# Performance work log

Hardware: AMD Instinct MI355X
Metric: run time of the kernel (lower is better)

Reference implementation:

```python
import jax, jax.numpy as jnp
import numpy as np

N_NODES = 100000
N_EDGES = 1600000
INPUT_DIM, HIDDEN_DIM, OUTPUT_DIM = 128, 256, 2
BN_EPS = 1e-5


def setup_inputs() -> dict:
    key = jax.random.key(0)
    ks = jax.random.split(key, 8)
    x = jax.random.normal(ks[0], (N_NODES, INPUT_DIM), jnp.float32)
    edge_index = jax.random.randint(ks[1], (2, N_EDGES), 0, N_NODES, dtype=jnp.int32).astype(jnp.int64)
    # Glorot-ish init for GCNConv weights; PyG GCNConv has bias by default.
    def glorot(k, fan_in, fan_out):
        s = jnp.sqrt(6.0 / (fan_in + fan_out))
        return jax.random.uniform(k, (fan_in, fan_out), jnp.float32, -s, s)
    return {
        "x": x,
        "edge_index": edge_index,
        "W0": glorot(ks[2], INPUT_DIM, HIDDEN_DIM),
        "b0": jnp.zeros((HIDDEN_DIM,), jnp.float32),
        "W1": glorot(ks[3], HIDDEN_DIM, HIDDEN_DIM),
        "b1": jnp.zeros((HIDDEN_DIM,), jnp.float32),
        "W2": glorot(ks[4], HIDDEN_DIM, OUTPUT_DIM),
        "b2": jnp.zeros((OUTPUT_DIM,), jnp.float32),
        "gamma0": jnp.ones((HIDDEN_DIM,), jnp.float32),
        "beta0": jnp.zeros((HIDDEN_DIM,), jnp.float32),
        "gamma1": jnp.ones((HIDDEN_DIM,), jnp.float32),
        "beta1": jnp.zeros((HIDDEN_DIM,), jnp.float32),
    }


def _gcn_norm(edge_index, num_nodes):
    # PyG gcn_norm: add self-loops, deg over destination, D^-1/2 A_hat D^-1/2
    loop = jnp.arange(num_nodes, dtype=edge_index.dtype)
    src = jnp.concatenate([edge_index[0], loop])
    dst = jnp.concatenate([edge_index[1], loop])
    deg = jax.ops.segment_sum(jnp.ones_like(dst, jnp.float32), dst, num_segments=num_nodes)
    dinv = jax.lax.rsqrt(jnp.maximum(deg, 1.0))  # deg >= 1 due to self-loops
    norm = dinv[src] * dinv[dst]  # [E + N]
    return src, dst, norm


def _gcn_conv(x, W, b, src, dst, norm, num_nodes):
    h = x @ W                          # [N, out] dense GEMM first (PyG order)
    msg = h[src] * norm[:, None]       # gather + edge scale
    out = jax.ops.segment_sum(msg, dst, num_segments=num_nodes)  # scatter-add
    return out + b


def _batchnorm(x, gamma, beta):
    # training-mode BatchNorm1d over nodes (biased variance, as torch uses for normalization)
    mean = jnp.mean(x, axis=0)
    var = jnp.mean(jnp.square(x - mean), axis=0)
    return (x - mean) * jax.lax.rsqrt(var + BN_EPS) * gamma + beta


def reference(x, edge_index, W0, b0, W1, b1, W2, b2, gamma0, beta0, gamma1, beta1):
    n = x.shape[0]
    src, dst, norm = _gcn_norm(edge_index, n)
    h = _gcn_conv(x, W0, b0, src, dst, norm, n)
    h = jax.nn.relu(_batchnorm(h, gamma0, beta0))  # dropout is identity (eval / deterministic)
    h = _gcn_conv(h, W1, b1, src, dst, norm, n)
    h = jax.nn.relu(_batchnorm(h, gamma1, beta1))
    out = _gcn_conv(h, W2, b2, src, dst, norm, n)
    return out
```

## Files before the change

kernel.cpp:

```cpp
#include <hip/hip_runtime.h>
#include <hip/hip_fp16.h>


#define BN_EPS 1e-5f

union HF4 { float4 f; __half2 h[4]; };

typedef __attribute__((ext_vector_type(8))) _Float16 f16x8;
typedef __attribute__((ext_vector_type(4))) float f32x4;

__global__ void detect_i64(const unsigned int* __restrict__ w, int* flag) {
  __shared__ unsigned int red[256];
  unsigned int v = 0;
  int t = threadIdx.x;
  for (int i = t; i < 1024; i += 256) v |= w[2 * i + 1];
  red[t] = v;
  __syncthreads();
  for (int s = 128; s > 0; s >>= 1) {
    if (t < s) red[t] |= red[t + s];
    __syncthreads();
  }
  if (t == 0) *flag = (red[0] == 0u) ? 1 : 0;
}

__global__ void convert_deg(const unsigned int* __restrict__ w, const int* __restrict__ flag,
                            int* __restrict__ srcI, int* __restrict__ dstI,
                            int* __restrict__ deg, int E) {
  int i = blockIdx.x * blockDim.x + threadIdx.x;
  if (i >= E) return;
  int f = *flag;
  int s = (int)(f ? w[2 * (size_t)i] : w[i]);
  int d = (int)(f ? w[2 * ((size_t)E + i)] : w[(size_t)E + i]);
  srcI[i] = s;
  dstI[i] = d;
  atomicAdd(&deg[d], 1);
}

__global__ void make_dinv(const int* __restrict__ deg, float* __restrict__ dinv,
                          float* __restrict__ stats, int N) {
  int i = blockIdx.x * blockDim.x + threadIdx.x;
  if (i < 512) stats[i] = 0.f;
  if (i < N) dinv[i] = rsqrtf((float)deg[i] + 1.0f);
}

__global__ void scan_partial(const int* __restrict__ deg, int* __restrict__ blksum, int N) {
  __shared__ int s[256];
  int b = blockIdx.x, t = threadIdx.x;
  int base = b * 1024 + t * 4;
  int v = 0;
#pragma unroll
  for (int k = 0; k < 4; ++k) {
    int i = base + k;
    if (i < N) v += deg[i];
  }
  s[t] = v;
  __syncthreads();
  for (int st = 128; st > 0; st >>= 1) {
    if (t < st) s[t] += s[t + st];
    __syncthreads();
  }
  if (t == 0) blksum[b] = s[0];
}

__global__ void scan_blk(int* __restrict__ blksum, int B) {
  __shared__ int s[256];
  int t = threadIdx.x;
  int v = (t < B) ? blksum[t] : 0;
  s[t] = v;
  __syncthreads();
  for (int off = 1; off < 256; off <<= 1) {
    int u = (t >= off) ? s[t - off] : 0;
    __syncthreads();
    s[t] += u;
    __syncthreads();
  }
  if (t < B) blksum[t] = s[t] - v;
}

__global__ void scan_final(const int* __restrict__ deg, const int* __restrict__ blkoff,
                           int* __restrict__ rowptr, int N, int E) {
  __shared__ int s[256];
  int b = blockIdx.x, t = threadIdx.x;
  int base = b * 1024 + t * 4;
  int v[4];
  int sum = 0;
#pragma unroll
  for (int k = 0; k < 4; ++k) {
    int i = base + k;
    v[k] = (i < N) ? deg[i] : 0;
    sum += v[k];
  }
  s[t] = sum;
  __syncthreads();
  for (int off = 1; off < 256; off <<= 1) {
    int u = (t >= off) ? s[t - off] : 0;
    __syncthreads();
    s[t] += u;
    __syncthreads();
  }
  int ex = s[t] - sum + blkoff[b];
#pragma unroll
  for (int k = 0; k < 4; ++k) {
    int i = base + k;
    if (i < N) {
      rowptr[i] = ex;
      ex += v[k];
    }
  }
  if (b == 0 && t == 0) rowptr[N] = E;
}

__global__ void csr_scatter(const int* __restrict__ src, const int* __restrict__ dst,
                            const float* __restrict__ dinv, const int* __restrict__ rowptr,
                            int* __restrict__ fill, int* __restrict__ col,
                            float* __restrict__ wgt, int E) {
  int e = blockIdx.x * blockDim.x + threadIdx.x;
  if (e >= E) return;
  int s = src[e], d = dst[e];
  int pos = atomicAdd(&fill[d], 1);
  int slot = rowptr[d] + pos;
  col[slot] = s;
  wgt[slot] = dinv[s] * dinv[d];
}

__global__ void f32_to_f16(const float4* __restrict__ in, float4* __restrict__ outh, long n8) {
  long t = (long)blockIdx.x * blockDim.x + threadIdx.x;
  if (t >= n8) return;
  float4 a = in[2 * t], b = in[2 * t + 1];
  HF4 o;
  o.h[0] = __floats2half2_rn(a.x, a.y);
  o.h[1] = __floats2half2_rn(a.z, a.w);
  o.h[2] = __floats2half2_rn(b.x, b.y);
  o.h[3] = __floats2half2_rn(b.z, b.w);
  outh[t] = o.f;
}

__global__ void pack_w(const float* __restrict__ W, _Float16* __restrict__ Wp, int K, int NC) {
  int idx = blockIdx.x * blockDim.x + threadIdx.x;
  if (idx >= K * NC) return;
  int k = idx / NC, n = idx - k * NC;
  int kb = k >> 5, kk = k & 31, seg = kk >> 3, j = kk & 7;
  Wp[(((kb * 4 + seg) * NC) + n) * 8 + j] = (_Float16)W[idx];
}

template <int LPN, bool BN>
__global__ void agg_gather_h(const float4* __restrict__ inh, float4* __restrict__ outh,
                             const int* __restrict__ rowptr, const int* __restrict__ col,
                             const float* __restrict__ wgt, const float* __restrict__ dinv,
                             const float* __restrict__ scale, const float* __restrict__ shift,
                             int N) {
  long g = (long)blockIdx.x * blockDim.x + threadIdx.x;
  int n = (int)(g / LPN);
  int lane = (int)(g & (LPN - 1));
  if (n >= N) return;
  float sc[8], sh[8];
  if (BN) {
    int c0 = lane * 8;
#pragma unroll
    for (int i = 0; i < 8; ++i) {
      sc[i] = scale[c0 + i];
      sh[i] = shift[c0 + i];
    }
  }
  auto xf = [&](const HF4& u, float* o) {
#pragma unroll
    for (int i = 0; i < 4; ++i) {
      float2 f = __half22float2(u.h[i]);
      o[2 * i] = f.x;
      o[2 * i + 1] = f.y;
    }
    if (BN) {
#pragma unroll
      for (int i = 0; i < 8; ++i) o[i] = fmaxf(o[i] * sc[i] + sh[i], 0.f);
    }
  };
  float ws = dinv[n];
  ws *= ws;
  float acc[8], v[8];
  {
    HF4 u;
    u.f = inh[(long)n * LPN + lane];
    xf(u, v);
#pragma unroll
    for (int i = 0; i < 8; ++i) acc[i] = ws * v[i];
  }
  int beg = rowptr[n], end = rowptr[n + 1];
  int j = beg;
  for (; j + 3 < end; j += 4) {
    int s0 = col[j], s1 = col[j + 1], s2 = col[j + 2], s3 = col[j + 3];
    float w0 = wgt[j], w1 = wgt[j + 1], w2 = wgt[j + 2], w3 = wgt[j + 3];
    HF4 a, b, c, d;
    a.f = inh[(long)s0 * LPN + lane];
    b.f = inh[(long)s1 * LPN + lane];
    c.f = inh[(long)s2 * LPN + lane];
    d.f = inh[(long)s3 * LPN + lane];
    float va[8], vb[8], vc[8], vd[8];
    xf(a, va); xf(b, vb); xf(c, vc); xf(d, vd);
#pragma unroll
    for (int i = 0; i < 8; ++i)
      acc[i] += w0 * va[i] + w1 * vb[i] + w2 * vc[i] + w3 * vd[i];
  }
  for (; j < end; ++j) {
    int s0 = col[j];
    float w0 = wgt[j];
    HF4 a;
    a.f = inh[(long)s0 * LPN + lane];
    float va[8];
    xf(a, va);
#pragma unroll
    for (int i = 0; i < 8; ++i) acc[i] += w0 * va[i];
  }
  HF4 o;
  o.h[0] = __floats2half2_rn(acc[0], acc[1]);
  o.h[1] = __floats2half2_rn(acc[2], acc[3]);
  o.h[2] = __floats2half2_rn(acc[4], acc[5]);
  o.h[3] = __floats2half2_rn(acc[6], acc[7]);
  outh[(long)n * LPN + lane] = o.f;
}

template <int K, int NC>
__global__ __launch_bounds__(256) void gemm_mfma(const _Float16* __restrict__ A,
                                                 const float4* __restrict__ Wpack,
                                                 _Float16* __restrict__ H,
                                                 float* __restrict__ gsum,
                                                 float* __restrict__ gsq, int M) {
  __shared__ float red0[NC];
  __shared__ float red1[NC];
  int tid = threadIdx.x;
  if (tid < NC) {
    red0[tid] = 0.f;
    red1[tid] = 0.f;
  }
  __syncthreads();
  int wave = tid >> 6;
  int lane = tid & 63;
  int row0 = (blockIdx.x * 4 + wave) * 32;
  bool active = row0 + 31 < M;
  int arow0 = active ? row0 : 0;
  int r = lane & 15;
  int seg = lane >> 4;
  f32x4 acc0[NC / 16], acc1[NC / 16];
#pragma unroll
  for (int t = 0; t < NC / 16; ++t) {
    acc0[t] = (f32x4){0.f, 0.f, 0.f, 0.f};
    acc1[t] = (f32x4){0.f, 0.f, 0.f, 0.f};
  }
  const _Float16* arowA = A + (long)(arow0 + r) * K;
  const _Float16* arowB = A + (long)(arow0 + 16 + r) * K;
#pragma unroll
  for (int k0 = 0; k0 < K; k0 += 32) {
    f16x8 af0 = *(const f16x8*)(arowA + k0 + seg * 8);
    f16x8 af1 = *(const f16x8*)(arowB + k0 + seg * 8);
    const float4* wp = Wpack + ((k0 >> 5) * 4 + seg) * NC;
#pragma unroll
    for (int t = 0; t < NC / 16; ++t) {
      f16x8 bf = *(const f16x8*)(wp + t * 16 + r);
      acc0[t] = __builtin_amdgcn_mfma_f32_16x16x32_f16(af0, bf, acc0[t], 0, 0, 0);
      acc1[t] = __builtin_amdgcn_mfma_f32_16x16x32_f16(af1, bf, acc1[t], 0, 0, 0);
    }
  }
#pragma unroll
  for (int t = 0; t < NC / 16; ++t) {
    int c = t * 16 + r;
    float s = 0.f, q = 0.f;
#pragma unroll
    for (int qq = 0; qq < 4; ++qq) {
      float v0 = acc0[t][qq], v1 = acc1[t][qq];
      s += v0 + v1;
      q += v0 * v0 + v1 * v1;
    }
    s += __shfl_xor(s, 16, 64);
    s += __shfl_xor(s, 32, 64);
    q += __shfl_xor(q, 16, 64);
    q += __shfl_xor(q, 32, 64);
    if (active) {
      if (seg == 0) {
        atomicAdd(&red0[c], s);
        atomicAdd(&red1[c], q);
      }
#pragma unroll
      for (int qq = 0; qq < 4; ++qq) {
        H[(long)(row0 + seg * 4 + qq) * NC + c] = (_Float16)acc0[t][qq];
        H[(long)(row0 + 16 + seg * 4 + qq) * NC + c] = (_Float16)acc1[t][qq];
      }
    }
  }
  __syncthreads();
  if (tid < NC) {
    atomicAdd(&gsum[tid], red0[tid]);
    atomicAdd(&gsq[tid], red1[tid]);
  }
}

__global__ void bn_finalize(float* __restrict__ gsum, float* __restrict__ gsq,
                            const float* __restrict__ gamma, const float* __restrict__ beta,
                            float* __restrict__ scale, float* __restrict__ shift, float invN) {
  int c = threadIdx.x;
  float mean = gsum[c] * invN;
  float var = fmaxf(gsq[c] * invN - mean * mean, 0.f);
  float sc = rsqrtf(var + BN_EPS) * gamma[c];
  scale[c] = sc;
  shift[c] = beta[c] - mean * sc;
  gsum[c] = 0.f;
  gsq[c] = 0.f;
}

__global__ void bn_apply_proj(const float4* __restrict__ h_in, const float* __restrict__ scale,
                              const float* __restrict__ shift, const float* __restrict__ W2,
                              float* __restrict__ P, int N) {
  int tid = threadIdx.x;
  int row = blockIdx.x * 8 + (tid >> 5);
  int lr = tid & 31;
  if (row >= N) return;
  HF4 u;
  u.f = h_in[(long)row * 32 + lr];
  int c0 = lr * 8;
  float s0 = 0.f, s1 = 0.f;
#pragma unroll
  for (int i = 0; i < 4; ++i) {
    float2 f = __half22float2(u.h[i]);
    int ca = c0 + 2 * i, cb = c0 + 2 * i + 1;
    float va = fmaxf(f.x * scale[ca] + shift[ca], 0.f);
    float vb = fmaxf(f.y * scale[cb] + shift[cb], 0.f);
    s0 += va * W2[2 * ca] + vb * W2[2 * cb];
    s1 += va * W2[2 * ca + 1] + vb * W2[2 * cb + 1];
  }
#pragma unroll
  for (int off = 16; off > 0; off >>= 1) {
    s0 += __shfl_down(s0, off, 32);
    s1 += __shfl_down(s1, off, 32);
  }
  if (lr == 0) {
    P[2 * row] = s0;
    P[2 * row + 1] = s1;
  }
}

__global__ void final_gather(const float* __restrict__ P, float* __restrict__ out,
                             const int* __restrict__ rowptr, const int* __restrict__ col,
                             const float* __restrict__ wgt, const float* __restrict__ dinv,
                             const float* __restrict__ b2, int N) {
  int n = blockIdx.x * blockDim.x + threadIdx.x;
  if (n >= N) return;
  float w = dinv[n] * dinv[n];
  float a0 = w * P[2 * n + 0];
  float a1 = w * P[2 * n + 1];
  int end = rowptr[n + 1];
  for (int j = rowptr[n]; j < end; ++j) {
    int s = col[j];
    float ww = wgt[j];
    a0 += ww * P[2 * s + 0];
    a1 += ww * P[2 * s + 1];
  }
  out[2 * n + 0] = a0 + b2[0];
  out[2 * n + 1] = a1 + b2[1];
}

extern "C" void kernel_launch(void* const* d_in, const int* in_sizes, int n_in,
                              void* d_out, int out_size, void* d_ws, size_t ws_size,
                              hipStream_t stream) {
  const float* x = (const float*)d_in[0];
  const unsigned int* eidx = (const unsigned int*)d_in[1];
  const float* W0 = (const float*)d_in[2];
  const float* W1 = (const float*)d_in[4];
  const float* W2 = (const float*)d_in[6];
  const float* b2 = (const float*)d_in[7];
  const float* gamma0 = (const float*)d_in[8];
  const float* beta0 = (const float*)d_in[9];
  const float* gamma1 = (const float*)d_in[10];
  const float* beta1 = (const float*)d_in[11];

  const int N = in_sizes[0] / 128;
  const int E = in_sizes[1] / 2;
  float* out = (float*)d_out;

  char* base = (char*)d_ws;
  size_t off = 0;
  auto alloc = [&](size_t bytes) {
    size_t o = off;
    off = (off + bytes + 255) & ~(size_t)255;
    return o;
  };
  const size_t o_col = alloc((size_t)E * 4);
  const size_t o_wgt = alloc((size_t)E * 4);
  const size_t o_rowptr = alloc((size_t)(N + 1) * 4);
  const size_t o_deg = alloc((size_t)N * 4);
  const size_t o_fill = alloc((size_t)N * 4);
  const size_t o_dinv = alloc((size_t)N * 4);
  const size_t o_blk = alloc(1024 * 4);
  const size_t o_flag = alloc(256);
  const size_t o_stats = alloc(4096);
  const size_t o_P = alloc((size_t)N * 2 * 4);
  const size_t o_W0p = alloc(128 * 256 * 2);
  const size_t o_W1p = alloc(256 * 256 * 2);
  const size_t o_H1 = alloc((size_t)N * 256 * 2);
  const size_t o_H2 = alloc((size_t)N * 256 * 2);

  int* col = (int*)(base + o_col);
  float* wgt = (float*)(base + o_wgt);
  int* rowptr = (int*)(base + o_rowptr);
  int* deg = (int*)(base + o_deg);
  int* fill = (int*)(base + o_fill);
  float* dinv = (float*)(base + o_dinv);
  int* blk = (int*)(base + o_blk);
  int* flag = (int*)(base + o_flag);
  float* gsum = (float*)(base + o_stats);
  float* gsq = gsum + 256;
  float* scale = gsum + 512;
  float* shift = gsum + 768;
  float* P = (float*)(base + o_P);
  _Float16* W0p = (_Float16*)(base + o_W0p);
  _Float16* W1p = (_Float16*)(base + o_W1p);
  float4* H1 = (float4*)(base + o_H1);
  float4* H2 = (float4*)(base + o_H2);
  int* idx32 = (int*)(base + o_H2);
  int* srcI = idx32;
  int* dstI = idx32 + E;

  auto cdiv = [](long a, long b) { return (int)((a + b - 1) / b); };
  const float invN = 1.0f / (float)N;
  const int B1 = cdiv(N, 1024);

  hipLaunchKernelGGL(detect_i64, dim3(1), dim3(256), 0, stream, eidx, flag);
  hipMemsetAsync(deg, 0, (size_t)N * 4, stream);
  hipMemsetAsync(fill, 0, (size_t)N * 4, stream);
  hipLaunchKernelGGL(convert_deg, dim3(cdiv(E, 256)), dim3(256), 0, stream, eidx, flag, srcI,
                     dstI, deg, E);

  hipLaunchKernelGGL(make_dinv, dim3(cdiv(N, 256)), dim3(256), 0, stream, deg, dinv, gsum, N);
  hipLaunchKernelGGL(scan_partial, dim3(B1), dim3(256), 0, stream, deg, blk, N);
  hipLaunchKernelGGL(scan_blk, dim3(1), dim3(256), 0, stream, blk, B1);
  hipLaunchKernelGGL(scan_final, dim3(B1), dim3(256), 0, stream, deg, blk, rowptr, N, E);
  hipLaunchKernelGGL(csr_scatter, dim3(cdiv(E, 256)), dim3(256), 0, stream, srcI, dstI, dinv,
                     rowptr, fill, col, wgt, E);
  hipLaunchKernelGGL(pack_w, dim3(cdiv(128 * 256, 256)), dim3(256), 0, stream, W0, W0p, 128, 256);
  hipLaunchKernelGGL(pack_w, dim3(cdiv(256 * 256, 256)), dim3(256), 0, stream, W1, W1p, 256, 256);
  hipLaunchKernelGGL(f32_to_f16, dim3(cdiv((long)N * 16, 256)), dim3(256), 0, stream,
                     (const float4*)x, H1, (long)N * 16);

  hipLaunchKernelGGL((agg_gather_h<16, false>), dim3(cdiv((long)N * 16, 256)), dim3(256), 0,
                     stream, H1, H2, rowptr, col, wgt, dinv, nullptr, nullptr, N);
  hipLaunchKernelGGL((gemm_mfma<128, 256>), dim3(cdiv(N, 128)), dim3(256), 0, stream,
                     (const _Float16*)H2, (const float4*)W0p, (_Float16*)H1, gsum, gsq, N);

  hipLaunchKernelGGL(bn_finalize, dim3(1), dim3(256), 0, stream, gsum, gsq, gamma0, beta0, scale,
                     shift, invN);

  hipLaunchKernelGGL((agg_gather_h<32, true>), dim3(cdiv((long)N * 32, 256)), dim3(256), 0,
                     stream, H1, H2, rowptr, col, wgt, dinv, scale, shift, N);
  hipLaunchKernelGGL((gemm_mfma<256, 256>), dim3(cdiv(N, 128)), dim3(256), 0, stream,
                     (const _Float16*)H2, (const float4*)W1p, (_Float16*)H1, gsum, gsq, N);

  hipLaunchKernelGGL(bn_finalize, dim3(1), dim3(256), 0, stream, gsum, gsq, gamma1, beta1, scale,
                     shift, invN);
  hipLaunchKernelGGL(bn_apply_proj, dim3(cdiv(N, 8)), dim3(256), 0, stream, (const float4*)H1,
                     scale, shift, W2, P, N);

  hipLaunchKernelGGL(final_gather, dim3(cdiv(N, 256)), dim3(256), 0, stream, P, out, rowptr, col,
                     wgt, dinv, b2, N);
}
```

Measured before the change: 557.3 us.

## Fuse CSR build passes, drop int32 index copies, and use grid-stride 8-deep gather

Removes the int32 src/dst staging arrays: degree counting reads only destinations, and the CSR scatter re-reads the raw edge index directly. The fill cursor is seeded with rowptr in the scan, so the scatter uses the atomic result as the slot and the separate fill memset goes away. The aggregation kernel becomes a grid-stride loop with a fixed block count, unrolls 8 neighbor loads to raise memory-level parallelism, and the 128-wide layer uses 32 lanes of 4 halves instead of 16 lanes of 8. The extra pass over the 64-bit edge index and the fixed grid size may offset some of the savings.

```diff
diff --git a/kernel.cpp b/kernel.cpp
--- a/kernel.cpp
+++ b/kernel.cpp
@@ -1,10 +1,12 @@
 #include <hip/hip_runtime.h>
 #include <hip/hip_fp16.h>
+#include <type_traits>
 
 
 #define BN_EPS 1e-5f
 
 union HF4 { float4 f; __half2 h[4]; };
+union HF2 { float2 f; __half2 h[2]; };
 
 typedef __attribute__((ext_vector_type(8))) _Float16 f16x8;
 typedef __attribute__((ext_vector_type(4))) float f32x4;
@@ -23,16 +25,12 @@
   if (t == 0) *flag = (red[0] == 0u) ? 1 : 0;
 }
 
-__global__ void convert_deg(const unsigned int* __restrict__ w, const int* __restrict__ flag,
-                            int* __restrict__ srcI, int* __restrict__ dstI,
-                            int* __restrict__ deg, int E) {
+__global__ void deg_count(const unsigned int* __restrict__ w, const int* __restrict__ flag,
+                          int* __restrict__ deg, int E) {
   int i = blockIdx.x * blockDim.x + threadIdx.x;
   if (i >= E) return;
   int f = *flag;
-  int s = (int)(f ? w[2 * (size_t)i] : w[i]);
   int d = (int)(f ? w[2 * ((size_t)E + i)] : w[(size_t)E + i]);
-  srcI[i] = s;
-  dstI[i] = d;
   atomicAdd(&deg[d], 1);
 }
 
@@ -78,7 +76,7 @@
 }
 
 __global__ void scan_final(const int* __restrict__ deg, const int* __restrict__ blkoff,
-                           int* __restrict__ rowptr, int N, int E) {
+                           int* __restrict__ rowptr, int* __restrict__ fill, int N, int E) {
   __shared__ int s[256];
   int b = blockIdx.x, t = threadIdx.x;
   int base = b * 1024 + t * 4;
@@ -104,21 +102,22 @@
     int i = base + k;
     if (i < N) {
       rowptr[i] = ex;
+      fill[i] = ex;
       ex += v[k];
     }
   }
   if (b == 0 && t == 0) rowptr[N] = E;
 }
 
-__global__ void csr_scatter(const int* __restrict__ src, const int* __restrict__ dst,
-                            const float* __restrict__ dinv, const int* __restrict__ rowptr,
-                            int* __restrict__ fill, int* __restrict__ col,
-                            float* __restrict__ wgt, int E) {
+__global__ void csr_scatter(const unsigned int* __restrict__ w, const int* __restrict__ flag,
+                            const float* __restrict__ dinv, int* __restrict__ fill,
+                            int* __restrict__ col, float* __restrict__ wgt, int E) {
   int e = blockIdx.x * blockDim.x + threadIdx.x;
   if (e >= E) return;
-  int s = src[e], d = dst[e];
-  int pos = atomicAdd(&fill[d], 1);
-  int slot = rowptr[d] + pos;
+  int f = *flag;
+  int s = (int)(f ? w[2 * (size_t)e] : w[e]);
+  int d = (int)(f ? w[2 * ((size_t)E + e)] : w[(size_t)E + e]);
+  int slot = atomicAdd(&fill[d], 1);
   col[slot] = s;
   wgt[slot] = dinv[s] * dinv[d];
 }
@@ -143,79 +142,105 @@
   Wp[(((kb * 4 + seg) * NC) + n) * 8 + j] = (_Float16)W[idx];
 }
 
-template <int LPN, bool BN>
-__global__ void agg_gather_h(const float4* __restrict__ inh, float4* __restrict__ outh,
+template <int LPN, int NH2, bool BN>
+__global__ void agg_gather_h(const _Float16* __restrict__ inh, _Float16* __restrict__ outh,
                              const int* __restrict__ rowptr, const int* __restrict__ col,
                              const float* __restrict__ wgt, const float* __restrict__ dinv,
                              const float* __restrict__ scale, const float* __restrict__ shift,
                              int N) {
-  long g = (long)blockIdx.x * blockDim.x + threadIdx.x;
-  int n = (int)(g / LPN);
-  int lane = (int)(g & (LPN - 1));
-  if (n >= N) return;
-  float sc[8], sh[8];
-  if (BN) {
-    int c0 = lane * 8;
-#pragma unroll
-    for (int i = 0; i < 8; ++i) {
-      sc[i] = scale[c0 + i];
-      sh[i] = shift[c0 + i];
-    }
-  }
-  auto xf = [&](const HF4& u, float* o) {
-#pragma unroll
-    for (int i = 0; i < 4; ++i) {
-      float2 f = __half22float2(u.h[i]);
-      o[2 * i] = f.x;
-      o[2 * i + 1] = f.y;
-    }
+  constexpr int NCH = NH2 * 2;
+  constexpr int ROWH = LPN * NCH;
+  using VT = typename std::conditional<NH2 == 4, float4, float2>::type;
+  using HU = typename std::conditional<NH2 == 4, HF4, HF2>::type;
+  long g0 = (long)blockIdx.x * blockDim.x + threadIdx.x;
+  long stride = (long)gridDim.x * blockDim.x;
+  long total = (long)N * LPN;
+  for (long g = g0; g < total; g += stride) {
+    int n = (int)(g >> 5);
+    int lane = (int)(g & (LPN - 1));
+    float sc[NCH], sh[NCH];
     if (BN) {
-#pragma unroll
-      for (int i = 0; i < 8; ++i) o[i] = fmaxf(o[i] * sc[i] + sh[i], 0.f);
-    }
-  };
-  float ws = dinv[n];
-  ws *= ws;
-  float acc[8], v[8];
-  {
-    HF4 u;
-    u.f = inh[(long)n * LPN + lane];
-    xf(u, v);
-#pragma unroll
-    for (int i = 0; i < 8; ++i) acc[i] = ws * v[i];
-  }
-  int beg = rowptr[n], end = rowptr[n + 1];
-  int j = beg;
-  for (; j + 3 < end; j += 4) {
-    int s0 = col[j], s1 = col[j + 1], s2 = col[j + 2], s3 = col[j + 3];
-    float w0 = wgt[j], w1 = wgt[j + 1], w2 = wgt[j + 2], w3 = wgt[j + 3];
-    HF4 a, b, c, d;
-    a.f = inh[(long)s0 * LPN + lane];
-    b.f = inh[(long)s1 * LPN + lane];
-    c.f = inh[(long)s2 * LPN + lane];
-    d.f = inh[(long)s3 * LPN + lane];
-    float va[8], vb[8], vc[8], vd[8];
-    xf(a, va); xf(b, vb); xf(c, vc); xf(d, vd);
-#pragma unroll
-    for (int i = 0; i < 8; ++i)
-      acc[i] += w0 * va[i] + w1 * vb[i] + w2 * vc[i] + w3 * vd[i];
-  }
-  for (; j < end; ++j) {
-    int s0 = col[j];
-    float w0 = wgt[j];
-    HF4 a;
-    a.f = inh[(long)s0 * LPN + lane];
-    float va[8];
-    xf(a, va);
-#pragma unroll
-    for (int i = 0; i < 8; ++i) acc[i] += w0 * va[i];
-  }
-  HF4 o;
-  o.h[0] = __floats2half2_rn(acc[0], acc[1]);
-  o.h[1] = __floats2half2_rn(acc[2], acc[3]);
-  o.h[2] = __floats2half2_rn(acc[4], acc[5]);
-  o.h[3] = __floats2half2_rn(acc[6], acc[7]);
-  outh[(long)n * LPN + lane] = o.f;
+      int c0 = lane * NCH;
+#pragma unroll
+      for (int i = 0; i < NCH; ++i) {
+        sc[i] = scale[c0 + i];
+        sh[i] = shift[c0 + i];
+      }
+    }
+    const _Float16* lanep = inh + lane * NCH;
+    auto xf = [&](HU u, float* o) {
+#pragma unroll
+      for (int i = 0; i < NH2; ++i) {
+        float2 f = __half22float2(u.h[i]);
+        o[2 * i] = f.x;
+        o[2 * i + 1] = f.y;
+      }
+      if (BN) {
+#pragma unroll
+        for (int i = 0; i < NCH; ++i) o[i] = fmaxf(o[i] * sc[i] + sh[i], 0.f);
+      }
+    };
+    float ws = dinv[n];
+    ws *= ws;
+    float acc[NCH];
+    {
+      HU u;
+      u.f = *(const VT*)(lanep + (long)n * ROWH);
+      float v[NCH];
+      xf(u, v);
+#pragma unroll
+      for (int i = 0; i < NCH; ++i) acc[i] = ws * v[i];
+    }
+    int j = rowptr[n], end = rowptr[n + 1];
+    for (; j + 7 < end; j += 8) {
+      HU u[8];
+      float w[8];
+#pragma unroll
+      for (int e = 0; e < 8; ++e) {
+        int s = col[j + e];
+        w[e] = wgt[j + e];
+        u[e].f = *(const VT*)(lanep + (long)s * ROWH);
+      }
+#pragma unroll
+      for (int e = 0; e < 8; ++e) {
+        float v[NCH];
+        xf(u[e], v);
+#pragma unroll
+        for (int i = 0; i < NCH; ++i) acc[i] += w[e] * v[i];
+      }
+    }
+    for (; j + 3 < end; j += 4) {
+      HU u[4];
+      float w[4];
+#pragma unroll
+      for (int e = 0; e < 4; ++e) {
+        int s = col[j + e];
+        w[e] = wgt[j + e];
+        u[e].f = *(const VT*)(lanep + (long)s * ROWH);
+      }
+#pragma unroll
+      for (int e = 0; e < 4; ++e) {
+        float v[NCH];
+        xf(u[e], v);
+#pragma unroll
+        for (int i = 0; i < NCH; ++i) acc[i] += w[e] * v[i];
+      }
+    }
+    for (; j < end; ++j) {
+      int s = col[j];
+      float w0 = wgt[j];
+      HU u;
+      u.f = *(const VT*)(lanep + (long)s * ROWH);
+      float v[NCH];
+      xf(u, v);
+#pragma unroll
+      for (int i = 0; i < NCH; ++i) acc[i] += w0 * v[i];
+    }
+    HU o;
+#pragma unroll
+    for (int i = 0; i < NH2; ++i) o.h[i] = __floats2half2_rn(acc[2 * i], acc[2 * i + 1]);
+    *(VT*)(outh + lane * NCH + (long)n * ROWH) = o.f;
+  }
 }
 
 template <int K, int NC>
@@ -411,45 +436,41 @@
   float* P = (float*)(base + o_P);
   _Float16* W0p = (_Float16*)(base + o_W0p);
   _Float16* W1p = (_Float16*)(base + o_W1p);
-  float4* H1 = (float4*)(base + o_H1);
-  float4* H2 = (float4*)(base + o_H2);
-  int* idx32 = (int*)(base + o_H2);
-  int* srcI = idx32;
-  int* dstI = idx32 + E;
+  _Float16* H1 = (_Float16*)(base + o_H1);
+  _Float16* H2 = (_Float16*)(base + o_H2);
 
   auto cdiv = [](long a, long b) { return (int)((a + b - 1) / b); };
   const float invN = 1.0f / (float)N;
   const int B1 = cdiv(N, 1024);
+  const int AGG_BLOCKS = 2048;
 
   hipLaunchKernelGGL(detect_i64, dim3(1), dim3(256), 0, stream, eidx, flag);
   hipMemsetAsync(deg, 0, (size_t)N * 4, stream);
-  hipMemsetAsync(fill, 0, (size_t)N * 4, stream);
-  hipLaunchKernelGGL(convert_deg, dim3(cdiv(E, 256)), dim3(256), 0, stream, eidx, flag, srcI,
-                     dstI, deg, E);
+  hipLaunchKernelGGL(deg_count, dim3(cdiv(E, 256)), dim3(256), 0, stream, eidx, flag, deg, E);
 
   hipLaunchKernelGGL(make_dinv, dim3(cdiv(N, 256)), dim3(256), 0, stream, deg, dinv, gsum, N);
   hipLaunchKernelGGL(scan_partial, dim3(B1), dim3(256), 0, stream, deg, blk, N);
   hipLaunchKernelGGL(scan_blk, dim3(1), dim3(256), 0, stream, blk, B1);
-  hipLaunchKernelGGL(scan_final, dim3(B1), dim3(256), 0, stream, deg, blk, rowptr, N, E);
-  hipLaunchKernelGGL(csr_scatter, dim3(cdiv(E, 256)), dim3(256), 0, stream, srcI, dstI, dinv,
-                     rowptr, fill, col, wgt, E);
+  hipLaunchKernelGGL(scan_final, dim3(B1), dim3(256), 0, stream, deg, blk, rowptr, fill, N, E);
+  hipLaunchKernelGGL(csr_scatter, dim3(cdiv(E, 256)), dim3(256), 0, stream, eidx, flag, dinv,
+                     fill, col, wgt, E);
   hipLaunchKernelGGL(pack_w, dim3(cdiv(128 * 256, 256)), dim3(256), 0, stream, W0, W0p, 128, 256);
   hipLaunchKernelGGL(pack_w, dim3(cdiv(256 * 256, 256)), dim3(256), 0, stream, W1, W1p, 256, 256);
   hipLaunchKernelGGL(f32_to_f16, dim3(cdiv((long)N * 16, 256)), dim3(256), 0, stream,
-                     (const float4*)x, H1, (long)N * 16);
-
-  hipLaunchKernelGGL((agg_gather_h<16, false>), dim3(cdiv((long)N * 16, 256)), dim3(256), 0,
-                     stream, H1, H2, rowptr, col, wgt, dinv, nullptr, nullptr, N);
+                     (const float4*)x, (float4*)H1, (long)N * 16);
+
+  hipLaunchKernelGGL((agg_gather_h<32, 2, false>), dim3(AGG_BLOCKS), dim3(256), 0, stream,
+                     H1, H2, rowptr, col, wgt, dinv, nullptr, nullptr, N);
   hipLaunchKernelGGL((gemm_mfma<128, 256>), dim3(cdiv(N, 128)), dim3(256), 0, stream,
-                     (const _Float16*)H2, (const float4*)W0p, (_Float16*)H1, gsum, gsq, N);
+                     H2, (const float4*)W0p, H1, gsum, gsq, N);
 
   hipLaunchKernelGGL(bn_finalize, dim3(1), dim3(256), 0, stream, gsum, gsq, gamma0, beta0, scale,
                      shift, invN);
 
-  hipLaunchKernelGGL((agg_gather_h<32, true>), dim3(cdiv((long)N * 32, 256)), dim3(256), 0,
-                     stream, H1, H2, rowptr, col, wgt, dinv, scale, shift, N);
+  hipLaunchKernelGGL((agg_gather_h<32, 4, true>), dim3(AGG_BLOCKS), dim3(256), 0, stream,
+                     H1, H2, rowptr, col, wgt, dinv, scale, shift, N);
   hipLaunchKernelGGL((gemm_mfma<256, 256>), dim3(cdiv(N, 128)), dim3(256), 0, stream,
-                     (const _Float16*)H2, (const float4*)W1p, (_Float16*)H1, gsum, gsq, N);
+                     H2, (const float4*)W1p, H1, gsum, gsq, N);
 
   hipLaunchKernelGGL(bn_finalize, dim3(1), dim3(256), 0, stream, gsum, gsq, gamma1, beta1, scale,
                      shift, invN);
```

After: 595.4 us. 6.8% more time.
